# Performance work log

Hardware: AMD Instinct MI355X
Metric: run time of the kernel (lower is better)

Reference implementation:

```python
import jax, jax.numpy as jnp
import numpy as np

# DeepSeek-V2-Lite MoE dims
E = 64      # n_routed_experts
H = 2048    # hidden_size
I = 1408    # moe_intermediate_size
K = 6       # num_experts_per_tok (top-k)
T = 1024    # tokens
C = 256     # per-expert capacity (expected load T*K/E = 96; 256 is ample, no drops with seed 0)


def setup_inputs() -> dict:
    key = jax.random.key(0)
    k1, k2, k3, k4 = jax.random.split(key, 4)
    return {
        "hidden_states": jax.random.normal(k1, (T, H), jnp.float32),
        "gate_w": jax.random.normal(k2, (H, E), jnp.float32) * 0.02,   # LiteLinear(H->E), no bias
        "w1": jax.random.normal(k3, (E, H, I), jnp.float32) * 0.02,    # experts_w1
        "w2": jax.random.normal(k4, (E, I, H), jnp.float32) * 0.02,    # experts_w2
    }


def _moe(x, gate_w, w1, w2):
    # Router: softmax gate + top-k + renormalize (vLLM fused_moe renormalize=True)
    logits = x @ gate_w                                    # [T, E]
    probs = jax.nn.softmax(logits, axis=-1)
    topk_w, topk_idx = jax.lax.top_k(probs, K)             # [T, K]
    topk_w = topk_w / jnp.sum(topk_w, axis=-1, keepdims=True)

    # Dispatch: flatten (token, k) pairs, compute slot position within each expert
    P = T * K
    e_p = topk_idx.reshape(P)                              # expert id per pair
    onehot = (e_p[:, None] == jnp.arange(E)[None, :]).astype(jnp.int32)  # [P, E]
    pos = jnp.cumsum(onehot, axis=0) - 1                   # running count per expert
    pos = jnp.take_along_axis(pos, e_p[:, None], axis=1)[:, 0]           # [P]
    valid = pos < C
    pos_c = jnp.where(valid, pos, 0)
    fvalid = valid[:, None].astype(x.dtype)

    x_pair = jnp.repeat(x, K, axis=0)                      # [P, H]
    xe = jnp.zeros((E, C, H), x.dtype).at[e_p, pos_c].add(x_pair * fvalid)  # [E, C, H]

    # Grouped expert GEMMs: silu(x @ w1) @ w2
    h = jax.nn.silu(jnp.einsum('ech,ehi->eci', xe, w1))    # [E, C, I]
    ye = jnp.einsum('eci,eih->ech', h, w2)                 # [E, C, H]

    # Combine: gather back per pair, weight by routing prob, sum over k
    y_pair = ye[e_p, pos_c] * fvalid                       # [P, H]
    out = (y_pair.reshape(T, K, H) * topk_w[..., None]).sum(axis=1)
    return out


def reference(hidden_states, gate_w, w1, w2):
    return _moe(hidden_states, gate_w, w1, w2)
```

## Files before the change

kernel.cpp:

```cpp
#include <hip/hip_runtime.h>

#define T_TOK 1024
#define H_DIM 2048
#define I_DIM 1408
#define E_NUM 64
#define K_TOP 6
#define CAP   256
#define P_NUM (T_TOK * K_TOP)

typedef __bf16 bf16x8 __attribute__((ext_vector_type(8)));
typedef float  f32x4  __attribute__((ext_vector_type(4)));
typedef unsigned int uint32x2 __attribute__((ext_vector_type(2)));

__device__ inline unsigned pack2bf16(float a, float b) {
    unsigned short au = __builtin_bit_cast(unsigned short, (__bf16)a);
    unsigned short bu = __builtin_bit_cast(unsigned short, (__bf16)b);
    return (unsigned)au | ((unsigned)bu << 16);
}

__global__ void zero_out_kernel(float* __restrict__ out) {
    int i = blockIdx.x * 256 + threadIdx.x;
    ((f32x4*)out)[i] = (f32x4){0.f, 0.f, 0.f, 0.f};
}

__global__ __launch_bounds__(256) void router_kernel(
        const float* __restrict__ x, const float* __restrict__ gw,
        float* __restrict__ tw, int* __restrict__ ti, __bf16* __restrict__ xb)
{
    const int t0  = blockIdx.x * 4;
    const int tid = threadIdx.x;
    __shared__ float xs[4][H_DIM];
    __shared__ float part[4][4][E_NUM];

    #pragma unroll
    for (int tt = 0; tt < 4; ++tt) {
        #pragma unroll
        for (int i = 0; i < 8; ++i) {
            float v = x[(size_t)(t0 + tt) * H_DIM + i * 256 + tid];
            xs[tt][i * 256 + tid] = v;
            xb[(size_t)(t0 + tt) * H_DIM + i * 256 + tid] = (__bf16)v;
        }
    }
    __syncthreads();

    const int e = tid & 63, q = tid >> 6;
    float a0 = 0.f, a1 = 0.f, a2 = 0.f, a3 = 0.f;
    for (int hh = q * 512; hh < q * 512 + 512; ++hh) {
        float g = gw[hh * E_NUM + e];
        a0 += xs[0][hh] * g; a1 += xs[1][hh] * g;
        a2 += xs[2][hh] * g; a3 += xs[3][hh] * g;
    }
    part[q][0][e] = a0; part[q][1][e] = a1; part[q][2][e] = a2; part[q][3][e] = a3;
    __syncthreads();

    const int tt = q;
    float l = part[0][tt][e] + part[1][tt][e] + part[2][tt][e] + part[3][tt][e];
    float m = l;
    #pragma unroll
    for (int s = 32; s; s >>= 1) m = fmaxf(m, __shfl_xor(m, s));
    float p = __expf(l - m);
    float sum = p;
    #pragma unroll
    for (int s = 32; s; s >>= 1) sum += __shfl_xor(sum, s);
    float prob = p / sum;

    float v = prob, wsum = 0.f;
    float tv[K_TOP]; int tix[K_TOP];
    #pragma unroll
    for (int k = 0; k < K_TOP; ++k) {
        float bv = v; int bi = e;
        #pragma unroll
        for (int s = 32; s; s >>= 1) {
            float ov = __shfl_xor(bv, s); int oi = __shfl_xor(bi, s);
            if (ov > bv || (ov == bv && oi < bi)) { bv = ov; bi = oi; }
        }
        tv[k] = bv; tix[k] = bi; wsum += bv;
        if (e == bi) v = -1.0f;
    }
    if (e == 0) {
        #pragma unroll
        for (int k = 0; k < K_TOP; ++k) {
            tw[(t0 + tt) * K_TOP + k] = tv[k] / wsum;
            ti[(t0 + tt) * K_TOP + k] = tix[k];
        }
    }
}

__global__ __launch_bounds__(1024) void dispatch_scan_kernel(
        const int* __restrict__ ti, int* __restrict__ cnt,
        int* __restrict__ base, int* __restrict__ list)
{
    __shared__ int lcnt[E_NUM];
    const int tid = threadIdx.x;
    if (tid < E_NUM) lcnt[tid] = 0;
    __syncthreads();
    #pragma unroll
    for (int i = 0; i < P_NUM / 1024; ++i) {
        int p = i * 1024 + tid;
        int e = ti[p];
        int slot = atomicAdd(&lcnt[e], 1);
        if (slot < CAP) list[e * CAP + slot] = p;
    }
    __syncthreads();
    if (tid == 0) {
        int acc = 0;
        for (int e = 0; e < E_NUM; ++e) {
            base[e] = acc;
            int c = lcnt[e];
            cnt[e] = c;
            if (c > CAP) c = CAP;
            acc += (c + 15) & ~15;
        }
    }
}

#define B_LDB 36

__global__ __launch_bounds__(256, 3) void gemm1_kernel(
        const float* __restrict__ w1, const __bf16* __restrict__ xb,
        const int* __restrict__ cnt, const int* __restrict__ base,
        const int* __restrict__ list, __bf16* __restrict__ hbuf)
{
    const int e  = blockIdx.z;
    const int m0 = blockIdx.y * 128;
    const int nb = blockIdx.x * 128;

    int rows = cnt[e]; if (rows > CAP) rows = CAP;
    const int rows_pad = (rows + 15) & ~15;
    if (m0 >= rows_pad) return;
    int mcount = rows_pad - m0; if (mcount > 128) mcount = 128;
    const int nmf = mcount >> 4;
    const int hb = base[e];

    __shared__ __attribute__((aligned(16))) __bf16 As[128][72];
    __shared__ __attribute__((aligned(16))) unsigned Bs[128 * B_LDB];
    __shared__ int ts[128];

    const int tid = threadIdx.x;
    if (tid < 128) {
        int slot = m0 + tid;
        ts[tid] = (slot < rows) ? (list[e * CAP + slot] / K_TOP) : 0;
    }
    __syncthreads();

    const int lane = tid & 63;
    const int wv   = tid >> 6;
    const int l15  = lane & 15;
    const int lg   = lane >> 4;

    const int sm = tid >> 3;
    const int sk = (tid & 7) << 3;
    const __bf16* ap[4];
    #pragma unroll
    for (int it = 0; it < 4; ++it)
        ap[it] = xb + (size_t)ts[it * 32 + sm] * H_DIM + sk;

    const int c4 = tid & 31;
    const int kb = tid >> 5;
    const int Xw = 4 * ((c4 ^ (c4 >> 3)) & 7);
    const float* bload = w1 + (size_t)e * H_DIM * I_DIM + (nb + 4 * c4);

    int cB0 = wv * 32 + l15;
    int cB1 = cB0 + 16;
    int c4r0 = cB0 >> 2, c4r1 = cB1 >> 2;
    const int Xr0 = 4 * ((c4r0 ^ (c4r0 >> 3)) & 7);
    const int Xr1 = 4 * ((c4r1 ^ (c4r1 >> 3)) & 7);
    const unsigned* bfp0 = Bs + cB0 * B_LDB;
    const unsigned* bfp1 = Bs + cB1 * B_LDB;

    f32x4 acc[8][2];
    #pragma unroll
    for (int m = 0; m < 8; ++m) {
        acc[m][0] = (f32x4){0.f, 0.f, 0.f, 0.f};
        acc[m][1] = (f32x4){0.f, 0.f, 0.f, 0.f};
    }

    f32x4 f[8]; bf16x8 av[4];
    {
        const float* bp = bload + (size_t)(4 * kb) * I_DIM;
        #pragma unroll
        for (int r = 0; r < 4; ++r) f[r] = *(const f32x4*)(bp + (size_t)r * I_DIM);
        const float* bp2 = bp + (size_t)32 * I_DIM;
        #pragma unroll
        for (int r = 0; r < 4; ++r) f[4 + r] = *(const f32x4*)(bp2 + (size_t)r * I_DIM);
        #pragma unroll
        for (int it = 0; it < 4; ++it) av[it] = *(const bf16x8*)(ap[it]);
    }

    for (int k0 = 0; k0 < H_DIM; k0 += 64) {
        int kn = k0 + 64; if (kn >= H_DIM) kn = 0;
        __syncthreads();
        #pragma unroll
        for (int it = 0; it < 4; ++it)
            *(bf16x8*)(&As[it * 32 + sm][sk]) = av[it];
        #pragma unroll
        for (int b = 0; b < 2; ++b) {
            #pragma unroll
            for (int i = 0; i < 4; ++i) {
                unsigned lo = pack2bf16(f[4 * b + 0][i], f[4 * b + 1][i]);
                unsigned hi = pack2bf16(f[4 * b + 2][i], f[4 * b + 3][i]);
                int c = 4 * c4 + i;
                int p = 2 * kb + 16 * b;
                *(uint32x2*)(&Bs[c * B_LDB + (p ^ Xw)]) = (uint32x2){lo, hi};
            }
        }
        {
            const float* bp = bload + (size_t)(kn + 4 * kb) * I_DIM;
            #pragma unroll
            for (int r = 0; r < 4; ++r) f[r] = *(const f32x4*)(bp + (size_t)r * I_DIM);
            const float* bp2 = bp + (size_t)32 * I_DIM;
            #pragma unroll
            for (int r = 0; r < 4; ++r) f[4 + r] = *(const f32x4*)(bp2 + (size_t)r * I_DIM);
            #pragma unroll
            for (int it = 0; it < 4; ++it) av[it] = *(const bf16x8*)(ap[it] + kn);
        }
        __syncthreads();
        #pragma unroll
        for (int ks = 0; ks < 2; ++ks) {
            int pbase = ks * 16 + lg * 4;
            bf16x8 b0 = *(const bf16x8*)(bfp0 + (pbase ^ Xr0));
            bf16x8 b1 = *(const bf16x8*)(bfp1 + (pbase ^ Xr1));
            #pragma unroll
            for (int m = 0; m < 8; ++m) {
                if (m < nmf) {
                    bf16x8 a = *(const bf16x8*)(&As[m * 16 + l15][ks * 32 + lg * 8]);
                    acc[m][0] = __builtin_amdgcn_mfma_f32_16x16x32_bf16(a, b0, acc[m][0], 0, 0, 0);
                    acc[m][1] = __builtin_amdgcn_mfma_f32_16x16x32_bf16(a, b1, acc[m][1], 0, 0, 0);
                }
            }
        }
    }

    const int nw = nb + wv * 32;
    #pragma unroll
    for (int m = 0; m < 8; ++m) {
        if (m < nmf) {
            #pragma unroll
            for (int nf = 0; nf < 2; ++nf) {
                #pragma unroll
                for (int j = 0; j < 4; ++j) {
                    int row = m * 16 + lg * 4 + j;
                    int col = nw + nf * 16 + l15;
                    float v = acc[m][nf][j];
                    float s = v / (1.0f + __expf(-v));
                    hbuf[(size_t)(hb + m0 + row) * I_DIM + col] = (__bf16)s;
                }
            }
        }
    }
}

__global__ __launch_bounds__(256, 3) void gemm2_kernel(
        const float* __restrict__ w2, const __bf16* __restrict__ hbuf,
        const int* __restrict__ cnt, const int* __restrict__ base,
        const int* __restrict__ list, const float* __restrict__ tw,
        float* __restrict__ out)
{
    const int e  = blockIdx.z;
    const int m0 = blockIdx.y * 128;
    const int nb = blockIdx.x * 128;

    int rows = cnt[e]; if (rows > CAP) rows = CAP;
    const int rows_pad = (rows + 15) & ~15;
    if (m0 >= rows_pad) return;
    int mcount = rows_pad - m0; if (mcount > 128) mcount = 128;
    const int nmf = mcount >> 4;
    const int hb = base[e];

    __shared__ __attribute__((aligned(16))) __bf16 As[128][72];
    __shared__ __attribute__((aligned(16))) unsigned Bs[128 * B_LDB];
    __shared__ int ps[128];
    __shared__ float tws[128];

    const int tid = threadIdx.x;
    if (tid < 128) {
        int slot = m0 + tid;
        int p = (slot < rows) ? list[e * CAP + slot] : -1;
        ps[tid] = p;
        tws[tid] = (p >= 0) ? tw[p] : 0.f;
    }

    const int lane = tid & 63;
    const int wv   = tid >> 6;
    const int l15  = lane & 15;
    const int lg   = lane >> 4;

    const int sm = tid >> 3;
    const int sk = (tid & 7) << 3;
    const __bf16* abase = hbuf + (size_t)(hb + m0 + sm) * I_DIM + sk;

    const int c4 = tid & 31;
    const int kb = tid >> 5;
    const int Xw = 4 * ((c4 ^ (c4 >> 3)) & 7);
    const float* bload = w2 + (size_t)e * I_DIM * H_DIM + (nb + 4 * c4);

    int cB0 = wv * 32 + l15;
    int cB1 = cB0 + 16;
    int c4r0 = cB0 >> 2, c4r1 = cB1 >> 2;
    const int Xr0 = 4 * ((c4r0 ^ (c4r0 >> 3)) & 7);
    const int Xr1 = 4 * ((c4r1 ^ (c4r1 >> 3)) & 7);
    const unsigned* bfp0 = Bs + cB0 * B_LDB;
    const unsigned* bfp1 = Bs + cB1 * B_LDB;

    f32x4 acc[8][2];
    #pragma unroll
    for (int m = 0; m < 8; ++m) {
        acc[m][0] = (f32x4){0.f, 0.f, 0.f, 0.f};
        acc[m][1] = (f32x4){0.f, 0.f, 0.f, 0.f};
    }

    f32x4 f[8]; bf16x8 av[4];
    {
        const float* bp = bload + (size_t)(4 * kb) * H_DIM;
        #pragma unroll
        for (int r = 0; r < 4; ++r) f[r] = *(const f32x4*)(bp + (size_t)r * H_DIM);
        const float* bp2 = bp + (size_t)32 * H_DIM;
        #pragma unroll
        for (int r = 0; r < 4; ++r) f[4 + r] = *(const f32x4*)(bp2 + (size_t)r * H_DIM);
        #pragma unroll
        for (int it = 0; it < 4; ++it)
            av[it] = *(const bf16x8*)(abase + (size_t)(it * 32) * I_DIM);
    }

    for (int k0 = 0; k0 < I_DIM; k0 += 64) {
        int kn = k0 + 64; if (kn >= I_DIM) kn = 0;
        __syncthreads();
        #pragma unroll
        for (int it = 0; it < 4; ++it)
            *(bf16x8*)(&As[it * 32 + sm][sk]) = av[it];
        #pragma unroll
        for (int b = 0; b < 2; ++b) {
            #pragma unroll
            for (int i = 0; i < 4; ++i) {
                unsigned lo = pack2bf16(f[4 * b + 0][i], f[4 * b + 1][i]);
                unsigned hi = pack2bf16(f[4 * b + 2][i], f[4 * b + 3][i]);
                int c = 4 * c4 + i;
                int p = 2 * kb + 16 * b;
                *(uint32x2*)(&Bs[c * B_LDB + (p ^ Xw)]) = (uint32x2){lo, hi};
            }
        }
        {
            const float* bp = bload + (size_t)(kn + 4 * kb) * H_DIM;
            #pragma unroll
            for (int r = 0; r < 4; ++r) f[r] = *(const f32x4*)(bp + (size_t)r * H_DIM);
            const float* bp2 = bp + (size_t)32 * H_DIM;
            #pragma unroll
            for (int r = 0; r < 4; ++r) f[4 + r] = *(const f32x4*)(bp2 + (size_t)r * H_DIM);
            #pragma unroll
            for (int it = 0; it < 4; ++it)
                av[it] = *(const bf16x8*)(abase + (size_t)(it * 32) * I_DIM + kn);
        }
        __syncthreads();

        #pragma unroll
        for (int ks = 0; ks < 2; ++ks) {
            int pbase = ks * 16 + lg * 4;
            bf16x8 b0 = *(const bf16x8*)(bfp0 + (pbase ^ Xr0));
            bf16x8 b1 = *(const bf16x8*)(bfp1 + (pbase ^ Xr1));
            #pragma unroll
            for (int m = 0; m < 8; ++m) {
                if (m < nmf) {
                    bf16x8 a = *(const bf16x8*)(&As[m * 16 + l15][ks * 32 + lg * 8]);
                    acc[m][0] = __builtin_amdgcn_mfma_f32_16x16x32_bf16(a, b0, acc[m][0], 0, 0, 0);
                    acc[m][1] = __builtin_amdgcn_mfma_f32_16x16x32_bf16(a, b1, acc[m][1], 0, 0, 0);
                }
            }
        }
    }

    const int nw = nb + wv * 32;
    #pragma unroll
    for (int m = 0; m < 8; ++m) {
        if (m < nmf) {
            #pragma unroll
            for (int nf = 0; nf < 2; ++nf) {
                #pragma unroll
                for (int j = 0; j < 4; ++j) {
                    int row = m * 16 + lg * 4 + j;
                    int p = ps[row];
                    if (p >= 0) {
                        int t = p / K_TOP;
                        float v = acc[m][nf][j] * tws[row];
                        atomicAdd(&out[(size_t)t * H_DIM + (nw + nf * 16 + l15)], v);
                    }
                }
            }
        }
    }
}

extern "C" void kernel_launch(void* const* d_in, const int* in_sizes, int n_in,
                              void* d_out, int out_size, void* d_ws, size_t ws_size,
                              hipStream_t stream) {
    const float* x  = (const float*)d_in[0];
    const float* gw = (const float*)d_in[1];
    const float* w1 = (const float*)d_in[2];
    const float* w2 = (const float*)d_in[3];
    float* out = (float*)d_out;

    char* ws = (char*)d_ws;
    int*    cnt  = (int*)ws;
    int*    base = (int*)(ws + 256);
    int*    list = (int*)(ws + 512);
    float*  tw   = (float*)(ws + 66048);
    int*    ti   = (int*)(ws + 90624);
    __bf16* xb   = (__bf16*)(ws + 131072);
    __bf16* hbuf = (__bf16*)(ws + 4325376);

    hipLaunchKernelGGL(zero_out_kernel, dim3(T_TOK * H_DIM / 4 / 256), dim3(256), 0, stream, out);
    hipLaunchKernelGGL(router_kernel, dim3(T_TOK / 4), dim3(256), 0, stream,
                       x, gw, tw, ti, xb);
    hipLaunchKernelGGL(dispatch_scan_kernel, dim3(1), dim3(1024), 0, stream,
                       ti, cnt, base, list);
    hipLaunchKernelGGL(gemm1_kernel, dim3(I_DIM / 128, 2, E_NUM), dim3(256), 0, stream,
                       w1, xb, cnt, base, list, hbuf);
    hipLaunchKernelGGL(gemm2_kernel, dim3(H_DIM / 128, 2, E_NUM), dim3(256), 0, stream,
                       w2, hbuf, cnt, base, list, tw, out);
}
```

Baseline: 448.8 us.

## Double-buffer LDS tiles with K-step 32 and one barrier per iteration

Both expert GEMM kernels now use a K-step of 32 instead of 64 and double-buffer the A and B shared-memory tiles. Each iteration writes into one buffer while the other is read, so the leading __syncthreads is dropped and only one barrier per step remains. The B-tile swizzle and stride are simplified to match the smaller tile, and prefetch registers are halved. The cost is twice as many loop iterations and barriers over the K dimension, each with less MFMA work per barrier.

After: 478.6 us. +6.6%, slower.

```diff
diff --git a/kernel.cpp b/kernel.cpp
--- a/kernel.cpp
+++ b/kernel.cpp
@@ -114,7 +114,7 @@
     }
 }
 
-#define B_LDB 36
+#define B_LDB 20
 
 __global__ __launch_bounds__(256, 3) void gemm1_kernel(
         const float* __restrict__ w1, const __bf16* __restrict__ xb,
@@ -132,8 +132,8 @@
     const int nmf = mcount >> 4;
     const int hb = base[e];
 
-    __shared__ __attribute__((aligned(16))) __bf16 As[128][72];
-    __shared__ __attribute__((aligned(16))) unsigned Bs[128 * B_LDB];
+    __shared__ __attribute__((aligned(16))) __bf16 As[2][128][40];
+    __shared__ __attribute__((aligned(16))) unsigned Bs[2][128 * B_LDB];
     __shared__ int ts[128];
 
     const int tid = threadIdx.x;
@@ -148,25 +148,20 @@
     const int l15  = lane & 15;
     const int lg   = lane >> 4;
 
-    const int sm = tid >> 3;
-    const int sk = (tid & 7) << 3;
-    const __bf16* ap[4];
-    #pragma unroll
-    for (int it = 0; it < 4; ++it)
-        ap[it] = xb + (size_t)ts[it * 32 + sm] * H_DIM + sk;
+    const int ar = tid >> 2;
+    const int ak = (tid & 3) << 3;
+    const __bf16* ap0 = xb + (size_t)ts[ar] * H_DIM + ak;
+    const __bf16* ap1 = xb + (size_t)ts[64 + ar] * H_DIM + ak;
 
     const int c4 = tid & 31;
     const int kb = tid >> 5;
-    const int Xw = 4 * ((c4 ^ (c4 >> 3)) & 7);
-    const float* bload = w1 + (size_t)e * H_DIM * I_DIM + (nb + 4 * c4);
-
-    int cB0 = wv * 32 + l15;
-    int cB1 = cB0 + 16;
-    int c4r0 = cB0 >> 2, c4r1 = cB1 >> 2;
-    const int Xr0 = 4 * ((c4r0 ^ (c4r0 >> 3)) & 7);
-    const int Xr1 = 4 * ((c4r1 ^ (c4r1 >> 3)) & 7);
-    const unsigned* bfp0 = Bs + cB0 * B_LDB;
-    const unsigned* bfp1 = Bs + cB1 * B_LDB;
+    const int Xw = 4 * (c4 & 3);
+    const float* bload = w1 + (size_t)e * H_DIM * I_DIM
+                            + (size_t)(4 * kb) * I_DIM + (nb + 4 * c4);
+
+    const int cB0 = wv * 32 + l15;
+    const int Xr  = 4 * ((l15 >> 2) & 3);
+    const int rb  = (lg * 4) ^ Xr;
 
     f32x4 acc[8][2];
     #pragma unroll
@@ -175,58 +170,42 @@
         acc[m][1] = (f32x4){0.f, 0.f, 0.f, 0.f};
     }
 
-    f32x4 f[8]; bf16x8 av[4];
-    {
-        const float* bp = bload + (size_t)(4 * kb) * I_DIM;
-        #pragma unroll
-        for (int r = 0; r < 4; ++r) f[r] = *(const f32x4*)(bp + (size_t)r * I_DIM);
-        const float* bp2 = bp + (size_t)32 * I_DIM;
-        #pragma unroll
-        for (int r = 0; r < 4; ++r) f[4 + r] = *(const f32x4*)(bp2 + (size_t)r * I_DIM);
-        #pragma unroll
-        for (int it = 0; it < 4; ++it) av[it] = *(const bf16x8*)(ap[it]);
-    }
-
-    for (int k0 = 0; k0 < H_DIM; k0 += 64) {
-        int kn = k0 + 64; if (kn >= H_DIM) kn = 0;
-        __syncthreads();
-        #pragma unroll
-        for (int it = 0; it < 4; ++it)
-            *(bf16x8*)(&As[it * 32 + sm][sk]) = av[it];
-        #pragma unroll
-        for (int b = 0; b < 2; ++b) {
-            #pragma unroll
-            for (int i = 0; i < 4; ++i) {
-                unsigned lo = pack2bf16(f[4 * b + 0][i], f[4 * b + 1][i]);
-                unsigned hi = pack2bf16(f[4 * b + 2][i], f[4 * b + 3][i]);
-                int c = 4 * c4 + i;
-                int p = 2 * kb + 16 * b;
-                *(uint32x2*)(&Bs[c * B_LDB + (p ^ Xw)]) = (uint32x2){lo, hi};
-            }
+    f32x4 f[4]; bf16x8 a0v, a1v;
+    #pragma unroll
+    for (int r = 0; r < 4; ++r) f[r] = *(const f32x4*)(bload + (size_t)r * I_DIM);
+    a0v = *(const bf16x8*)(ap0);
+    a1v = *(const bf16x8*)(ap1);
+
+    const int NSTEP = H_DIM / 32;
+    for (int t = 0; t < NSTEP; ++t) {
+        const int buf = t & 1;
+        *(bf16x8*)(&As[buf][ar][ak])      = a0v;
+        *(bf16x8*)(&As[buf][64 + ar][ak]) = a1v;
+        #pragma unroll
+        for (int i = 0; i < 4; ++i) {
+            unsigned lo = pack2bf16(f[0][i], f[1][i]);
+            unsigned hi = pack2bf16(f[2][i], f[3][i]);
+            *(uint32x2*)(&Bs[buf][(4 * c4 + i) * B_LDB + ((2 * kb) ^ Xw)]) =
+                (uint32x2){lo, hi};
         }
         {
-            const float* bp = bload + (size_t)(kn + 4 * kb) * I_DIM;
+            int kn = (t + 1 < NSTEP) ? (t + 1) * 32 : 0;
+            const float* bp = bload + (size_t)kn * I_DIM;
             #pragma unroll
             for (int r = 0; r < 4; ++r) f[r] = *(const f32x4*)(bp + (size_t)r * I_DIM);
-            const float* bp2 = bp + (size_t)32 * I_DIM;
-            #pragma unroll
-            for (int r = 0; r < 4; ++r) f[4 + r] = *(const f32x4*)(bp2 + (size_t)r * I_DIM);
-            #pragma unroll
-            for (int it = 0; it < 4; ++it) av[it] = *(const bf16x8*)(ap[it] + kn);
+            a0v = *(const bf16x8*)(ap0 + kn);
+            a1v = *(const bf16x8*)(ap1 + kn);
         }
         __syncthreads();
-        #pragma unroll
-        for (int ks = 0; ks < 2; ++ks) {
-            int pbase = ks * 16 + lg * 4;
-            bf16x8 b0 = *(const bf16x8*)(bfp0 + (pbase ^ Xr0));
-            bf16x8 b1 = *(const bf16x8*)(bfp1 + (pbase ^ Xr1));
-            #pragma unroll
-            for (int m = 0; m < 8; ++m) {
-                if (m < nmf) {
-                    bf16x8 a = *(const bf16x8*)(&As[m * 16 + l15][ks * 32 + lg * 8]);
-                    acc[m][0] = __builtin_amdgcn_mfma_f32_16x16x32_bf16(a, b0, acc[m][0], 0, 0, 0);
-                    acc[m][1] = __builtin_amdgcn_mfma_f32_16x16x32_bf16(a, b1, acc[m][1], 0, 0, 0);
-                }
+        const unsigned* bcol = &Bs[buf][cB0 * B_LDB];
+        bf16x8 b0 = *(const bf16x8*)(bcol + rb);
+        bf16x8 b1 = *(const bf16x8*)(bcol + 16 * B_LDB + rb);
+        #pragma unroll
+        for (int m = 0; m < 8; ++m) {
+            if (m < nmf) {
+                bf16x8 a = *(const bf16x8*)(&As[buf][m * 16 + l15][lg * 8]);
+                acc[m][0] = __builtin_amdgcn_mfma_f32_16x16x32_bf16(a, b0, acc[m][0], 0, 0, 0);
+                acc[m][1] = __builtin_amdgcn_mfma_f32_16x16x32_bf16(a, b1, acc[m][1], 0, 0, 0);
             }
         }
     }
@@ -267,8 +246,8 @@
     const int nmf = mcount >> 4;
     const int hb = base[e];
 
-    __shared__ __attribute__((aligned(16))) __bf16 As[128][72];
-    __shared__ __attribute__((aligned(16))) unsigned Bs[128 * B_LDB];
+    __shared__ __attribute__((aligned(16))) __bf16 As[2][128][40];
+    __shared__ __attribute__((aligned(16))) unsigned Bs[2][128 * B_LDB];
     __shared__ int ps[128];
     __shared__ float tws[128];
 
@@ -285,22 +264,20 @@
     const int l15  = lane & 15;
     const int lg   = lane >> 4;
 
-    const int sm = tid >> 3;
-    const int sk = (tid & 7) << 3;
-    const __bf16* abase = hbuf + (size_t)(hb + m0 + sm) * I_DIM + sk;
+    const int ar = tid >> 2;
+    const int ak = (tid & 3) << 3;
+    const __bf16* ap0 = hbuf + (size_t)(hb + m0 + ar) * I_DIM + ak;
+    const __bf16* ap1 = hbuf + (size_t)(hb + m0 + 64 + ar) * I_DIM + ak;
 
     const int c4 = tid & 31;
     const int kb = tid >> 5;
-    const int Xw = 4 * ((c4 ^ (c4 >> 3)) & 7);
-    const float* bload = w2 + (size_t)e * I_DIM * H_DIM + (nb + 4 * c4);
-
-    int cB0 = wv * 32 + l15;
-    int cB1 = cB0 + 16;
-    int c4r0 = cB0 >> 2, c4r1 = cB1 >> 2;
-    const int Xr0 = 4 * ((c4r0 ^ (c4r0 >> 3)) & 7);
-    const int Xr1 = 4 * ((c4r1 ^ (c4r1 >> 3)) & 7);
-    const unsigned* bfp0 = Bs + cB0 * B_LDB;
-    const unsigned* bfp1 = Bs + cB1 * B_LDB;
+    const int Xw = 4 * (c4 & 3);
+    const float* bload = w2 + (size_t)e * I_DIM * H_DIM
+                            + (size_t)(4 * kb) * H_DIM + (nb + 4 * c4);
+
+    const int cB0 = wv * 32 + l15;
+    const int Xr  = 4 * ((l15 >> 2) & 3);
+    const int rb  = (lg * 4) ^ Xr;
 
     f32x4 acc[8][2];
     #pragma unroll
@@ -309,61 +286,42 @@
         acc[m][1] = (f32x4){0.f, 0.f, 0.f, 0.f};
     }
 
-    f32x4 f[8]; bf16x8 av[4];
-    {
-        const float* bp = bload + (size_t)(4 * kb) * H_DIM;
-        #pragma unroll
-        for (int r = 0; r < 4; ++r) f[r] = *(const f32x4*)(bp + (size_t)r * H_DIM);
-        const float* bp2 = bp + (size_t)32 * H_DIM;
-        #pragma unroll
-        for (int r = 0; r < 4; ++r) f[4 + r] = *(const f32x4*)(bp2 + (size_t)r * H_DIM);
-        #pragma unroll
-        for (int it = 0; it < 4; ++it)
-            av[it] = *(const bf16x8*)(abase + (size_t)(it * 32) * I_DIM);
-    }
-
-    for (int k0 = 0; k0 < I_DIM; k0 += 64) {
-        int kn = k0 + 64; if (kn >= I_DIM) kn = 0;
-        __syncthreads();
-        #pragma unroll
-        for (int it = 0; it < 4; ++it)
-            *(bf16x8*)(&As[it * 32 + sm][sk]) = av[it];
-        #pragma unroll
-        for (int b = 0; b < 2; ++b) {
-            #pragma unroll
-            for (int i = 0; i < 4; ++i) {
-                unsigned lo = pack2bf16(f[4 * b + 0][i], f[4 * b + 1][i]);
-                unsigned hi = pack2bf16(f[4 * b + 2][i], f[4 * b + 3][i]);
-                int c = 4 * c4 + i;
-                int p = 2 * kb + 16 * b;
-                *(uint32x2*)(&Bs[c * B_LDB + (p ^ Xw)]) = (uint32x2){lo, hi};
-            }
+    f32x4 f[4]; bf16x8 a0v, a1v;
+    #pragma unroll
+    for (int r = 0; r < 4; ++r) f[r] = *(const f32x4*)(bload + (size_t)r * H_DIM);
+    a0v = *(const bf16x8*)(ap0);
+    a1v = *(const bf16x8*)(ap1);
+
+    const int NSTEP = I_DIM / 32;
+    for (int t = 0; t < NSTEP; ++t) {
+        const int buf = t & 1;
+        *(bf16x8*)(&As[buf][ar][ak])      = a0v;
+        *(bf16x8*)(&As[buf][64 + ar][ak]) = a1v;
+        #pragma unroll
+        for (int i = 0; i < 4; ++i) {
+            unsigned lo = pack2bf16(f[0][i], f[1][i]);
+            unsigned hi = pack2bf16(f[2][i], f[3][i]);
+            *(uint32x2*)(&Bs[buf][(4 * c4 + i) * B_LDB + ((2 * kb) ^ Xw)]) =
+                (uint32x2){lo, hi};
         }
         {
-            const float* bp = bload + (size_t)(kn + 4 * kb) * H_DIM;
+            int kn = (t + 1 < NSTEP) ? (t + 1) * 32 : 0;
+            const float* bp = bload + (size_t)kn * H_DIM;
             #pragma unroll
             for (int r = 0; r < 4; ++r) f[r] = *(const f32x4*)(bp + (size_t)r * H_DIM);
-            const float* bp2 = bp + (size_t)32 * H_DIM;
-            #pragma unroll
-            for (int r = 0; r < 4; ++r) f[4 + r] = *(const f32x4*)(bp2 + (size_t)r * H_DIM);
-            #pragma unroll
-            for (int it = 0; it < 4; ++it)
-                av[it] = *(const bf16x8*)(abase + (size_t)(it * 32) * I_DIM + kn);
+            a0v = *(const bf16x8*)(ap0 + kn);
+            a1v = *(const bf16x8*)(ap1 + kn);
         }
         __syncthreads();
-
-        #pragma unroll
-        for (int ks = 0; ks < 2; ++ks) {
-            int pbase = ks * 16 + lg * 4;
-            bf16x8 b0 = *(const bf16x8*)(bfp0 + (pbase ^ Xr0));
-            bf16x8 b1 = *(const bf16x8*)(bfp1 + (pbase ^ Xr1));
-            #pragma unroll
-            for (int m = 0; m < 8; ++m) {
-                if (m < nmf) {
-                    bf16x8 a = *(const bf16x8*)(&As[m * 16 + l15][ks * 32 + lg * 8]);
-                    acc[m][0] = __builtin_amdgcn_mfma_f32_16x16x32_bf16(a, b0, acc[m][0], 0, 0, 0);
-                    acc[m][1] = __builtin_amdgcn_mfma_f32_16x16x32_bf16(a, b1, acc[m][1], 0, 0, 0);
-                }
+        const unsigned* bcol = &Bs[buf][cB0 * B_LDB];
+        bf16x8 b0 = *(const bf16x8*)(bcol + rb);
+        bf16x8 b1 = *(const bf16x8*)(bcol + 16 * B_LDB + rb);
+        #pragma unroll
+        for (int m = 0; m < 8; ++m) {
+            if (m < nmf) {
+                bf16x8 a = *(const bf16x8*)(&As[buf][m * 16 + l15][lg * 8]);
+                acc[m][0] = __builtin_amdgcn_mfma_f32_16x16x32_bf16(a, b0, acc[m][0], 0, 0, 0);
+                acc[m][1] = __builtin_amdgcn_mfma_f32_16x16x32_bf16(a, b1, acc[m][1], 0, 0, 0);
             }
         }
     }
```
